# Kernel optimization log

Hardware: AMD Instinct MI355X
Metric: run time of the kernel (lower is better)

## Reference

```python
import jax, jax.numpy as jnp
import numpy as np

N, D, K, MAX_ITER = 131072, 64, 512, 5


def setup_inputs() -> dict:
    key = jax.random.key(0)
    k1, k2, k3 = jax.random.split(key, 3)
    X = jax.random.normal(k1, (N, D), dtype=jnp.float32)
    centers = jax.random.normal(k2, (K, D), dtype=jnp.float32)
    repl_idx = jax.random.randint(k3, (MAX_ITER, K), 0, N, dtype=jnp.int32)
    return {"X": X, "centers": centers, "repl_idx": repl_idx}


def _assign(X, centers):
    # squared euclidean distance matrix [N, K]; argmin identical to cdist argmin
    x2 = jnp.sum(X * X, axis=1, keepdims=True)          # [N,1]
    c2 = jnp.sum(centers * centers, axis=1)             # [K]
    d2 = x2 + c2[None, :] - 2.0 * (X @ centers.T)       # [N,K]
    return jnp.argmin(d2, axis=1)


def reference(X, centers, repl_idx):
    n_clusters = centers.shape[0]
    assignments = None
    for i in range(MAX_ITER):
        assignments = _assign(X, centers)
        # scatter_mean: per-cluster sum / count (empty clusters -> 0, as torch_scatter)
        sums = jax.ops.segment_sum(X, assignments, num_segments=n_clusters)
        counts = jax.ops.segment_sum(jnp.ones((X.shape[0],), X.dtype), assignments,
                                     num_segments=n_clusters)
        new_centers = sums / jnp.maximum(counts, 1.0)[:, None]
        # re-initialize any exactly-zero entries from random data points
        new_centers_init = X[repl_idx[i]]                 # [K,D]
        new_centers = jnp.where(new_centers == 0, new_centers_init, new_centers)
        centers = new_centers
    return assignments, centers
```

## Files before the change

### kernel.cpp

```cpp
#include <hip/hip_runtime.h>

#define N_PTS 131072
#define KC    512
#define DIM   64
#define MAXIT 5
#define NCHUNK 64
#define CHUNK_PTS (N_PTS / NCHUNK)
#define FIXSCALE 1099511627776.0

typedef short v8s __attribute__((ext_vector_type(8)));
typedef float v4f __attribute__((ext_vector_type(4)));

__device__ __forceinline__ unsigned short bf16_rtne(float x) {
    unsigned int u = __float_as_uint(x);
    return (unsigned short)((u + 0x7FFFu + ((u >> 16) & 1u)) >> 16);
}
__device__ __forceinline__ float bf16_f32(unsigned short b) {
    return __uint_as_float(((unsigned int)b) << 16);
}
__device__ __forceinline__ void split3(float x, short& h, short& m, short& l) {
    unsigned short hb = bf16_rtne(x);
    float r1 = x - bf16_f32(hb);
    unsigned short mb = bf16_rtne(r1);
    float r2 = r1 - bf16_f32(mb);
    h = (short)hb; m = (short)mb; l = (short)bf16_rtne(r2);
}

__global__ __launch_bounds__(256) void prep_kernel(
        const float* __restrict__ C, float* __restrict__ c2out,
        unsigned short* __restrict__ Ch, unsigned short* __restrict__ Cm,
        unsigned short* __restrict__ Cl) {
    int k = blockIdx.x * 256 + threadIdx.x;
    if (k < KC) {
        float sq[DIM];
        #pragma unroll
        for (int j = 0; j < DIM; ++j) {
            float c = C[k * DIM + j];
            sq[j] = c * c;
            short h, m, l;
            split3(c, h, m, l);
            Ch[k * DIM + j] = (unsigned short)h;
            Cm[k * DIM + j] = (unsigned short)m;
            Cl[k * DIM + j] = (unsigned short)l;
        }
        #pragma unroll
        for (int st = 1; st < DIM; st <<= 1)
            #pragma unroll
            for (int j = 0; j < DIM; j += 2 * st)
                sq[j] = sq[j] + sq[j + st];
        c2out[k] = sq[0];
    }
}

__global__ __launch_bounds__(256, 4) void assign_kernel(
        const float* __restrict__ X,
        const unsigned short* __restrict__ Ch,
        const unsigned short* __restrict__ Cm,
        const unsigned short* __restrict__ Cl,
        const float* __restrict__ c2v, float* __restrict__ out_f) {
    __shared__ short Bt[6 * 64 * 8];
    __shared__ float c2t[KC];
    __shared__ float x2p[4][2][16][8];
    __shared__ float x2f[4][2][16];

    const int t   = threadIdx.x;
    const int wv  = t >> 6;
    const int l   = t & 63;
    const int row = l & 15;
    const int q   = l >> 4;
    const int pbase = blockIdx.x * 128 + wv * 32;

    for (int i = t; i < KC; i += 256) c2t[i] = c2v[i];

    v8s ah[2][2], am[2][2], al[2][2];
    #pragma unroll
    for (int T = 0; T < 2; ++T) {
        const float* xr = X + (size_t)(pbase + T * 16 + row) * DIM + q * 8;
        #pragma unroll
        for (int kc = 0; kc < 2; ++kc) {
            float4 v0 = *(const float4*)(xr + kc * 32);
            float4 v1 = *(const float4*)(xr + kc * 32 + 4);
            float e[8] = { v0.x, v0.y, v0.z, v0.w, v1.x, v1.y, v1.z, v1.w };
            v8s H, M, L;
            #pragma unroll
            for (int j = 0; j < 8; ++j) {
                short hh, mm, ll;
                split3(e[j], hh, mm, ll);
                H[j] = hh; M[j] = mm; L[j] = ll;
            }
            ah[T][kc] = H; am[T][kc] = M; al[T][kc] = L;
            float s0 = e[0]*e[0], s1 = e[1]*e[1], s2 = e[2]*e[2], s3 = e[3]*e[3];
            float s4 = e[4]*e[4], s5 = e[5]*e[5], s6 = e[6]*e[6], s7 = e[7]*e[7];
            x2p[wv][T][row][kc * 4 + q] =
                ((s0 + s1) + (s2 + s3)) + ((s4 + s5) + (s6 + s7));
        }
    }
    __syncthreads();
    if (t < 128) {
        int w2 = t >> 5, T2 = (t >> 4) & 1, pt = t & 15;
        const float* P = x2p[w2][T2][pt];
        x2f[w2][T2][pt] = ((P[0] + P[1]) + (P[2] + P[3]))
                        + ((P[4] + P[5]) + (P[6] + P[7]));
    }
    __syncthreads();
    float x2x[2][4];
    #pragma unroll
    for (int T = 0; T < 2; ++T)
        #pragma unroll
        for (int r = 0; r < 4; ++r)
            x2x[T][r] = x2f[wv][T][q * 4 + r];

    float bd[2][4];
    int   bk[2][4];
    #pragma unroll
    for (int T = 0; T < 2; ++T)
        #pragma unroll
        for (int r = 0; r < 4; ++r) { bd[T][r] = 3.4e38f; bk[T][r] = 0; }

    const unsigned short* const bases[3] = { Ch, Cm, Cl };
    #define CHUNK_GPTR(c, ct) ((const v8s*)(bases[(c) >> 7] +                 \
        ((size_t)((ct) * 16 + (((c) & 63) & 15)) * 64 +                       \
         (((c) >> 6) & 1) * 32 + (((c) & 63) >> 4) * 8)))

    v8s r1 = *CHUNK_GPTR(t, 0);
    v8s r2;
    if (t < 128) r2 = *CHUNK_GPTR(256 + t, 0);

    v8s* const BtV = (v8s*)Bt;
    for (int ct = 0; ct < 32; ++ct) {
        __syncthreads();
        BtV[t] = r1;
        if (t < 128) BtV[256 + t] = r2;
        if (ct < 31) {
            r1 = *CHUNK_GPTR(t, ct + 1);
            if (t < 128) r2 = *CHUNK_GPTR(256 + t, ct + 1);
        }
        __syncthreads();

        v8s bh0 = BtV[0 * 64 + l];
        v8s bh1 = BtV[1 * 64 + l];
        v8s bm0 = BtV[2 * 64 + l];
        v8s bm1 = BtV[3 * 64 + l];
        v8s bl0 = BtV[4 * 64 + l];
        v8s bl1 = BtV[5 * 64 + l];
        float c2k = c2t[ct * 16 + row];

        #pragma unroll
        for (int T = 0; T < 2; ++T) {
            v4f acc = {0.f, 0.f, 0.f, 0.f};
            acc = __builtin_amdgcn_mfma_f32_16x16x32_bf16(ah[T][0], bh0, acc, 0, 0, 0);
            acc = __builtin_amdgcn_mfma_f32_16x16x32_bf16(ah[T][1], bh1, acc, 0, 0, 0);
            acc = __builtin_amdgcn_mfma_f32_16x16x32_bf16(am[T][0], bh0, acc, 0, 0, 0);
            acc = __builtin_amdgcn_mfma_f32_16x16x32_bf16(am[T][1], bh1, acc, 0, 0, 0);
            acc = __builtin_amdgcn_mfma_f32_16x16x32_bf16(ah[T][0], bm0, acc, 0, 0, 0);
            acc = __builtin_amdgcn_mfma_f32_16x16x32_bf16(ah[T][1], bm1, acc, 0, 0, 0);
            acc = __builtin_amdgcn_mfma_f32_16x16x32_bf16(am[T][0], bm0, acc, 0, 0, 0);
            acc = __builtin_amdgcn_mfma_f32_16x16x32_bf16(am[T][1], bm1, acc, 0, 0, 0);
            acc = __builtin_amdgcn_mfma_f32_16x16x32_bf16(al[T][0], bh0, acc, 0, 0, 0);
            acc = __builtin_amdgcn_mfma_f32_16x16x32_bf16(al[T][1], bh1, acc, 0, 0, 0);
            acc = __builtin_amdgcn_mfma_f32_16x16x32_bf16(ah[T][0], bl0, acc, 0, 0, 0);
            acc = __builtin_amdgcn_mfma_f32_16x16x32_bf16(ah[T][1], bl1, acc, 0, 0, 0);
            #pragma unroll
            for (int r = 0; r < 4; ++r) {
                float tt = x2x[T][r] + c2k;
                float d2 = fmaf(-2.0f, acc[r], tt);
                if (d2 < bd[T][r]) { bd[T][r] = d2; bk[T][r] = ct * 16 + row; }
            }
        }
    }
    #undef CHUNK_GPTR

    #pragma unroll
    for (int T = 0; T < 2; ++T)
        #pragma unroll
        for (int r = 0; r < 4; ++r) {
            unsigned int b = __float_as_uint(bd[T][r]);
            b = (b & 0x80000000u) ? ~b : (b | 0x80000000u);
            unsigned long long key = ((unsigned long long)b << 32)
                                   | (unsigned int)bk[T][r];
            #pragma unroll
            for (int st = 1; st <= 8; st <<= 1) {
                unsigned long long o = __shfl_xor(key, st, 64);
                if (o < key) key = o;
            }
            if (row == 0) {
                int p = pbase + T * 16 + q * 4 + r;
                out_f[p] = (float)((int)(unsigned int)key);
            }
        }
}

__global__ __launch_bounds__(256) void accum_kernel(
        const float* __restrict__ X, const float* __restrict__ af,
        unsigned long long* __restrict__ qsums, int* __restrict__ counts) {
    __shared__ unsigned long long lsum[KC * 16];
    __shared__ int lcnt[KC];
    int slice = blockIdx.x & 3;
    int chunk = blockIdx.x >> 2;
    int p4 = threadIdx.x >> 2;
    int c4 = threadIdx.x & 3;

    for (int i = threadIdx.x; i < KC * 16; i += 256) lsum[i] = 0ull;
    for (int i = threadIdx.x; i < KC; i += 256) lcnt[i] = 0;
    __syncthreads();

    int base = chunk * CHUNK_PTS;
    #pragma unroll 2
    for (int it = 0; it < CHUNK_PTS / 64; ++it) {
        int n = base + it * 64 + p4;
        int a = (int)af[n];
        float4 xv = *(const float4*)(X + (size_t)n * DIM + slice * 16 + c4 * 4);
        long long q0 = (long long)llrint((double)xv.x * FIXSCALE);
        long long q1 = (long long)llrint((double)xv.y * FIXSCALE);
        long long q2 = (long long)llrint((double)xv.z * FIXSCALE);
        long long q3 = (long long)llrint((double)xv.w * FIXSCALE);
        atomicAdd(&lsum[a * 16 + c4 * 4 + 0], (unsigned long long)q0);
        atomicAdd(&lsum[a * 16 + c4 * 4 + 1], (unsigned long long)q1);
        atomicAdd(&lsum[a * 16 + c4 * 4 + 2], (unsigned long long)q2);
        atomicAdd(&lsum[a * 16 + c4 * 4 + 3], (unsigned long long)q3);
        if (slice == 0 && c4 == 0) atomicAdd(&lcnt[a], 1);
    }
    __syncthreads();

    for (int i = threadIdx.x; i < KC * 16; i += 256) {
        unsigned long long v = lsum[i];
        if (v != 0ull)
            atomicAdd(&qsums[(i >> 4) * DIM + slice * 16 + (i & 15)], v);
    }
    if (slice == 0)
        for (int i = threadIdx.x; i < KC; i += 256) {
            int v = lcnt[i];
            if (v != 0) atomicAdd(&counts[i], v);
        }
}

__global__ __launch_bounds__(256) void update_kernel(
        const unsigned long long* __restrict__ qsums,
        const int* __restrict__ counts,
        const int* __restrict__ repl, const float* __restrict__ X,
        float* __restrict__ outC, float* __restrict__ c2v,
        unsigned short* __restrict__ Ch, unsigned short* __restrict__ Cm,
        unsigned short* __restrict__ Cl) {
    int k = blockIdx.x * 4 + (threadIdx.x >> 6);
    int d = threadIdx.x & 63;

    long long qq = (long long)qsums[k * DIM + d];
    float s = (float)((double)qq * (1.0 / FIXSCALE));
    float cnt = (float)counts[k];
    float v = s / fmaxf(cnt, 1.0f);
    if (v == 0.0f) v = X[(size_t)repl[k] * DIM + d];
    outC[k * DIM + d] = v;

    short h, m, l;
    split3(v, h, m, l);
    Ch[k * DIM + d] = (unsigned short)h;
    Cm[k * DIM + d] = (unsigned short)m;
    Cl[k * DIM + d] = (unsigned short)l;

    float sq = v * v;
    #pragma unroll
    for (int st = 1; st < 64; st <<= 1)
        sq += __shfl_xor(sq, st, 64);
    if (d == 0) c2v[k] = sq;
}

extern "C" void kernel_launch(void* const* d_in, const int* in_sizes, int n_in,
                              void* d_out, int out_size, void* d_ws, size_t ws_size,
                              hipStream_t stream) {
    const float* X    = (const float*)d_in[0];
    const float* C0   = (const float*)d_in[1];
    const int*   repl = (const int*)d_in[2];
    float* out = (float*)d_out;

    char* ws = (char*)d_ws;
    unsigned short* Ch = (unsigned short*)(ws + 0);
    unsigned short* Cm = (unsigned short*)(ws + (64 << 10));
    unsigned short* Cl = (unsigned short*)(ws + (128 << 10));
    unsigned long long* qsums = (unsigned long long*)(ws + (192 << 10));
    int*   counts = (int*)  (ws + (448 << 10));
    float* c2v    = (float*)(ws + (450 << 10));

    prep_kernel<<<2, 256, 0, stream>>>(C0, c2v, Ch, Cm, Cl);

    for (int i = 0; i < MAXIT; ++i) {
        assign_kernel<<<N_PTS / 128, 256, 0, stream>>>(
            X, Ch, Cm, Cl, c2v, out);

        hipMemsetAsync(qsums, 0, KC * DIM * sizeof(unsigned long long)
                                 + KC * sizeof(int), stream);

        accum_kernel<<<NCHUNK * 4, 256, 0, stream>>>(X, out, qsums, counts);

        update_kernel<<<KC / 4, 256, 0, stream>>>(
            qsums, counts, repl + i * KC, X, out + N_PTS, c2v, Ch, Cm, Cl);
    }
}
```

Before: 469.1 us.

## Double-buffer center tiles in LDS, two tiles per stage, one barrier per step

Measured after the change: 716.4 us. +52.7%, slower.

```diff
diff --git a/kernel.cpp b/kernel.cpp
--- a/kernel.cpp
+++ b/kernel.cpp
@@ -58,7 +58,7 @@
         const unsigned short* __restrict__ Cm,
         const unsigned short* __restrict__ Cl,
         const float* __restrict__ c2v, float* __restrict__ out_f) {
-    __shared__ short Bt[6 * 64 * 8];
+    __shared__ __align__(16) short Bt[2 * 12 * 64 * 8];
     __shared__ float c2t[KC];
     __shared__ float x2p[4][2][16][8];
     __shared__ float x2f[4][2][16];
@@ -69,6 +69,23 @@
     const int row = l & 15;
     const int q   = l >> 4;
     const int pbase = blockIdx.x * 128 + wv * 32;
+
+    const unsigned short* const bases[3] = { Ch, Cm, Cl };
+    auto slot_ptr = [&](int i) -> const unsigned short* {
+        int half = (i >= 384) ? 1 : 0;
+        int c = i - half * 384;
+        return bases[c >> 7]
+             + (size_t)((half * 16 + (c & 15)) * 64
+                        + ((c >> 6) & 1) * 32 + ((c & 63) >> 4) * 8);
+    };
+    const unsigned short* p0 = slot_ptr(t);
+    const unsigned short* p1 = slot_ptr(256 + t);
+    const unsigned short* p2 = slot_ptr(512 + t);
+
+    v8s r0 = *(const v8s*)p0;
+    v8s r1 = *(const v8s*)p1;
+    v8s r2 = *(const v8s*)p2;
+    __builtin_amdgcn_sched_barrier(0);
 
     for (int i = t; i < KC; i += 256) c2t[i] = c2v[i];
 
@@ -95,6 +112,13 @@
                 ((s0 + s1) + (s2 + s3)) + ((s4 + s5) + (s6 + s7));
         }
     }
+
+    v8s* const BtV = (v8s*)Bt;
+    BtV[t] = r0; BtV[256 + t] = r1; BtV[512 + t] = r2;
+    r0 = *(const v8s*)(p0 + 2048);
+    r1 = *(const v8s*)(p1 + 2048);
+    r2 = *(const v8s*)(p2 + 2048);
+
     __syncthreads();
     if (t < 128) {
         int w2 = t >> 5, T2 = (t >> 4) & 1, pt = t & 15;
@@ -117,58 +141,61 @@
         #pragma unroll
         for (int r = 0; r < 4; ++r) { bd[T][r] = 3.4e38f; bk[T][r] = 0; }
 
-    const unsigned short* const bases[3] = { Ch, Cm, Cl };
-    #define CHUNK_GPTR(c, ct) ((const v8s*)(bases[(c) >> 7] +                 \
-        ((size_t)((ct) * 16 + (((c) & 63) & 15)) * 64 +                       \
-         (((c) >> 6) & 1) * 32 + (((c) & 63) >> 4) * 8)))
-
-    v8s r1 = *CHUNK_GPTR(t, 0);
-    v8s r2;
-    if (t < 128) r2 = *CHUNK_GPTR(256 + t, 0);
-
-    v8s* const BtV = (v8s*)Bt;
-    for (int ct = 0; ct < 32; ++ct) {
-        __syncthreads();
-        BtV[t] = r1;
-        if (t < 128) BtV[256 + t] = r2;
-        if (ct < 31) {
-            r1 = *CHUNK_GPTR(t, ct + 1);
-            if (t < 128) r2 = *CHUNK_GPTR(256 + t, ct + 1);
-        }
-        __syncthreads();
-
-        v8s bh0 = BtV[0 * 64 + l];
-        v8s bh1 = BtV[1 * 64 + l];
-        v8s bm0 = BtV[2 * 64 + l];
-        v8s bm1 = BtV[3 * 64 + l];
-        v8s bl0 = BtV[4 * 64 + l];
-        v8s bl1 = BtV[5 * 64 + l];
-        float c2k = c2t[ct * 16 + row];
-
-        #pragma unroll
-        for (int T = 0; T < 2; ++T) {
-            v4f acc = {0.f, 0.f, 0.f, 0.f};
-            acc = __builtin_amdgcn_mfma_f32_16x16x32_bf16(ah[T][0], bh0, acc, 0, 0, 0);
-            acc = __builtin_amdgcn_mfma_f32_16x16x32_bf16(ah[T][1], bh1, acc, 0, 0, 0);
-            acc = __builtin_amdgcn_mfma_f32_16x16x32_bf16(am[T][0], bh0, acc, 0, 0, 0);
-            acc = __builtin_amdgcn_mfma_f32_16x16x32_bf16(am[T][1], bh1, acc, 0, 0, 0);
-            acc = __builtin_amdgcn_mfma_f32_16x16x32_bf16(ah[T][0], bm0, acc, 0, 0, 0);
-            acc = __builtin_amdgcn_mfma_f32_16x16x32_bf16(ah[T][1], bm1, acc, 0, 0, 0);
-            acc = __builtin_amdgcn_mfma_f32_16x16x32_bf16(am[T][0], bm0, acc, 0, 0, 0);
-            acc = __builtin_amdgcn_mfma_f32_16x16x32_bf16(am[T][1], bm1, acc, 0, 0, 0);
-            acc = __builtin_amdgcn_mfma_f32_16x16x32_bf16(al[T][0], bh0, acc, 0, 0, 0);
-            acc = __builtin_amdgcn_mfma_f32_16x16x32_bf16(al[T][1], bh1, acc, 0, 0, 0);
-            acc = __builtin_amdgcn_mfma_f32_16x16x32_bf16(ah[T][0], bl0, acc, 0, 0, 0);
-            acc = __builtin_amdgcn_mfma_f32_16x16x32_bf16(ah[T][1], bl1, acc, 0, 0, 0);
+    const unsigned short* q0 = p0 + 2 * 2048;
+    const unsigned short* q1 = p1 + 2 * 2048;
+    const unsigned short* q2p = p2 + 2 * 2048;
+
+    #pragma unroll 2
+    for (int it = 0; it < 16; ++it) {
+        const int cur = it & 1;
+        v8s* const rbuf = BtV + cur * 768;
+        if (it < 15) {
+            v8s* const wbuf = BtV + (cur ^ 1) * 768;
+            wbuf[t] = r0; wbuf[256 + t] = r1; wbuf[512 + t] = r2;
+        }
+        if (it < 14) {
+            r0 = *(const v8s*)q0;  q0  += 2048;
+            r1 = *(const v8s*)q1;  q1  += 2048;
+            r2 = *(const v8s*)q2p; q2p += 2048;
+        }
+        __builtin_amdgcn_sched_barrier(0);
+
+        #pragma unroll
+        for (int half = 0; half < 2; ++half) {
+            const int tile = 2 * it + half;
+            v8s bh0 = rbuf[half * 384 + 0 * 64 + l];
+            v8s bh1 = rbuf[half * 384 + 1 * 64 + l];
+            v8s bm0 = rbuf[half * 384 + 2 * 64 + l];
+            v8s bm1 = rbuf[half * 384 + 3 * 64 + l];
+            v8s bl0 = rbuf[half * 384 + 4 * 64 + l];
+            v8s bl1 = rbuf[half * 384 + 5 * 64 + l];
+            float c2k = c2t[tile * 16 + row];
+
             #pragma unroll
-            for (int r = 0; r < 4; ++r) {
-                float tt = x2x[T][r] + c2k;
-                float d2 = fmaf(-2.0f, acc[r], tt);
-                if (d2 < bd[T][r]) { bd[T][r] = d2; bk[T][r] = ct * 16 + row; }
+            for (int T = 0; T < 2; ++T) {
+                v4f acc = {0.f, 0.f, 0.f, 0.f};
+                acc = __builtin_amdgcn_mfma_f32_16x16x32_bf16(ah[T][0], bh0, acc, 0, 0, 0);
+                acc = __builtin_amdgcn_mfma_f32_16x16x32_bf16(ah[T][1], bh1, acc, 0, 0, 0);
+                acc = __builtin_amdgcn_mfma_f32_16x16x32_bf16(am[T][0], bh0, acc, 0, 0, 0);
+                acc = __builtin_amdgcn_mfma_f32_16x16x32_bf16(am[T][1], bh1, acc, 0, 0, 0);
+                acc = __builtin_amdgcn_mfma_f32_16x16x32_bf16(ah[T][0], bm0, acc, 0, 0, 0);
+                acc = __builtin_amdgcn_mfma_f32_16x16x32_bf16(ah[T][1], bm1, acc, 0, 0, 0);
+                acc = __builtin_amdgcn_mfma_f32_16x16x32_bf16(am[T][0], bm0, acc, 0, 0, 0);
+                acc = __builtin_amdgcn_mfma_f32_16x16x32_bf16(am[T][1], bm1, acc, 0, 0, 0);
+                acc = __builtin_amdgcn_mfma_f32_16x16x32_bf16(al[T][0], bh0, acc, 0, 0, 0);
+                acc = __builtin_amdgcn_mfma_f32_16x16x32_bf16(al[T][1], bh1, acc, 0, 0, 0);
+                acc = __builtin_amdgcn_mfma_f32_16x16x32_bf16(ah[T][0], bl0, acc, 0, 0, 0);
+                acc = __builtin_amdgcn_mfma_f32_16x16x32_bf16(ah[T][1], bl1, acc, 0, 0, 0);
+                #pragma unroll
+                for (int r = 0; r < 4; ++r) {
+                    float tt = x2x[T][r] + c2k;
+                    float d2 = fmaf(-2.0f, acc[r], tt);
+                    if (d2 < bd[T][r]) { bd[T][r] = d2; bk[T][r] = tile * 16 + row; }
+                }
             }
         }
-    }
-    #undef CHUNK_GPTR
+        if (it < 15) __syncthreads();
+    }
 
     #pragma unroll
     for (int T = 0; T < 2; ++T)
```

## Double-buffer center tiles in LDS via direct global-to-LDS loads

Applied to the files above, without the earlier changes.

After: 473.6 us. No clear change (+0.9%).

```diff
diff --git a/kernel.cpp b/kernel.cpp
--- a/kernel.cpp
+++ b/kernel.cpp
@@ -24,6 +24,13 @@
     unsigned short mb = bf16_rtne(r1);
     float r2 = r1 - bf16_f32(mb);
     h = (short)hb; m = (short)mb; l = (short)bf16_rtne(r2);
+}
+
+__device__ __forceinline__ void gload_lds16(const unsigned short* g, void* lds) {
+    __builtin_amdgcn_global_load_lds(
+        (const __attribute__((address_space(1))) void*)g,
+        (__attribute__((address_space(3))) void*)lds,
+        16, 0, 0);
 }
 
 __global__ __launch_bounds__(256) void prep_kernel(
@@ -58,7 +65,7 @@
         const unsigned short* __restrict__ Cm,
         const unsigned short* __restrict__ Cl,
         const float* __restrict__ c2v, float* __restrict__ out_f) {
-    __shared__ short Bt[6 * 64 * 8];
+    __shared__ __align__(16) short Bt[2 * 6 * 64 * 8];
     __shared__ float c2t[KC];
     __shared__ float x2p[4][2][16][8];
     __shared__ float x2f[4][2][16];
@@ -69,6 +76,18 @@
     const int row = l & 15;
     const int q   = l >> 4;
     const int pbase = blockIdx.x * 128 + wv * 32;
+
+    const unsigned short* const gsrc1 =
+        ((wv < 2) ? Ch : Cm) + (size_t)(row * 64 + (wv & 1) * 32 + q * 8);
+    const unsigned short* const gsrc2 =
+        Cl + (size_t)(row * 64 + wv * 32 + q * 8);
+
+    v8s* const BtV = (v8s*)Bt;
+    v8s* const lds1 = BtV + wv * 64;
+    v8s* const lds2 = BtV + 256 + wv * 64;
+
+    gload_lds16(gsrc1, lds1);
+    if (wv < 2) gload_lds16(gsrc2, lds2);
 
     for (int i = t; i < KC; i += 256) c2t[i] = c2v[i];
 
@@ -117,32 +136,20 @@
         #pragma unroll
         for (int r = 0; r < 4; ++r) { bd[T][r] = 3.4e38f; bk[T][r] = 0; }
 
-    const unsigned short* const bases[3] = { Ch, Cm, Cl };
-    #define CHUNK_GPTR(c, ct) ((const v8s*)(bases[(c) >> 7] +                 \
-        ((size_t)((ct) * 16 + (((c) & 63) & 15)) * 64 +                       \
-         (((c) >> 6) & 1) * 32 + (((c) & 63) >> 4) * 8)))
-
-    v8s r1 = *CHUNK_GPTR(t, 0);
-    v8s r2;
-    if (t < 128) r2 = *CHUNK_GPTR(256 + t, 0);
-
-    v8s* const BtV = (v8s*)Bt;
     for (int ct = 0; ct < 32; ++ct) {
-        __syncthreads();
-        BtV[t] = r1;
-        if (t < 128) BtV[256 + t] = r2;
+        const int cur = ct & 1;
         if (ct < 31) {
-            r1 = *CHUNK_GPTR(t, ct + 1);
-            if (t < 128) r2 = *CHUNK_GPTR(256 + t, ct + 1);
-        }
-        __syncthreads();
-
-        v8s bh0 = BtV[0 * 64 + l];
-        v8s bh1 = BtV[1 * 64 + l];
-        v8s bm0 = BtV[2 * 64 + l];
-        v8s bm1 = BtV[3 * 64 + l];
-        v8s bl0 = BtV[4 * 64 + l];
-        v8s bl1 = BtV[5 * 64 + l];
+            const size_t goff = (size_t)(ct + 1) * 1024;
+            gload_lds16(gsrc1 + goff, lds1 + (cur ^ 1) * 384);
+            if (wv < 2) gload_lds16(gsrc2 + goff, lds2 + (cur ^ 1) * 384);
+        }
+        v8s* const rb = BtV + cur * 384;
+        v8s bh0 = rb[0 * 64 + l];
+        v8s bh1 = rb[1 * 64 + l];
+        v8s bm0 = rb[2 * 64 + l];
+        v8s bm1 = rb[3 * 64 + l];
+        v8s bl0 = rb[4 * 64 + l];
+        v8s bl1 = rb[5 * 64 + l];
         float c2k = c2t[ct * 16 + row];
 
         #pragma unroll
@@ -167,8 +174,8 @@
                 if (d2 < bd[T][r]) { bd[T][r] = d2; bk[T][r] = ct * 16 + row; }
             }
         }
-    }
-    #undef CHUNK_GPTR
+        if (ct < 31) __syncthreads();
+    }
 
     #pragma unroll
     for (int T = 0; T < 2; ++T)
```
